# Optimization experiments

Measured on AMD Instinct MI355X. Metric: run time of the kernel, lower is better.

The kernel has to match this reference:

```python
import jax, jax.numpy as jnp
import numpy as np

IMG_C = 256
GC = 32  # graph_channel; must equal graph feature dim 32 for the residual


def setup_inputs() -> dict:
    key = jax.random.key(0)
    ks = jax.random.split(key, 10)
    B, N, WH_SIDE = 8, 4096, 64
    s = lambda fan_in: 1.0 / np.sqrt(fan_in)
    return {
        "input_graph": jax.random.normal(ks[0], (B, N, GC), jnp.float32),
        "input_image": jax.random.normal(ks[1], (B, IMG_C, WH_SIDE, WH_SIDE), jnp.float32),
        # Conv1d(kernel=1) weights stored as [out, in]
        "Wq": jax.random.uniform(ks[2], (GC, 32), jnp.float32, -s(32), s(32)),
        "bq": jax.random.uniform(ks[3], (GC,), jnp.float32, -s(32), s(32)),
        "Wk": jax.random.uniform(ks[4], (GC, IMG_C), jnp.float32, -s(IMG_C), s(IMG_C)),
        "bk": jax.random.uniform(ks[5], (GC,), jnp.float32, -s(IMG_C), s(IMG_C)),
        "Wv": jax.random.uniform(ks[6], (GC, IMG_C), jnp.float32, -s(IMG_C), s(IMG_C)),
        "bv": jax.random.uniform(ks[7], (GC,), jnp.float32, -s(IMG_C), s(IMG_C)),
        "Wc": jax.random.uniform(ks[8], (GC, GC), jnp.float32, -s(GC), s(GC)),
        "bc": jax.random.uniform(ks[9], (GC,), jnp.float32, -s(GC), s(GC)),
    }


def reference(input_graph, input_image, Wq, bq, Wk, bk, Wv, bv, Wc, bc):
    B, C, W, H = input_image.shape
    img = input_image.reshape(B, C, W * H)                      # [B, C, L]
    # 1x1 conv projections == channel matmuls
    K = jnp.einsum('oc,bcl->bol', Wk, img) + bk[None, :, None]  # [B, GC, L]
    V = jnp.einsum('oc,bcl->bol', Wv, img) + bv[None, :, None]  # [B, GC, L]
    # Q: graph [B, N, 32] -> conv over channel dim -> [B, N, GC]
    Q = jnp.einsum('oc,bnc->bno', Wq, input_graph) + bq[None, None, :]
    att = jnp.einsum('bno,bol->bnl', Q, K) / jnp.sqrt(jnp.float32(GC))  # [B, N, L]
    # NOTE: original softmax is over dim=1 (the node/query axis)
    att = jax.nn.softmax(att, axis=1)
    message = jnp.einsum('bol,bnl->bon', V, att)                # [B, GC, N]
    out = input_graph.transpose(0, 2, 1) + (
        jnp.einsum('oc,bcn->bon', Wc, message) + bc[None, :, None]
    )                                                           # [B, GC, N]
    return out.transpose(0, 2, 1)                               # [B, N, GC]
```

## Files before the change

kernel.cpp:

```cpp
#include <hip/hip_runtime.h>

#define BB 8
#define NN 4096
#define LL 4096
#define CC 256

typedef short bf16x8 __attribute__((ext_vector_type(8)));
typedef _Float16 f16x8 __attribute__((ext_vector_type(8)));
typedef __fp16 hf16x2 __attribute__((ext_vector_type(2)));
typedef float f32x4 __attribute__((ext_vector_type(4)));

__device__ __forceinline__ float bf2f(short s) {
  union { unsigned u; float f; } v;
  v.u = ((unsigned)(unsigned short)s) << 16;
  return v.f;
}
__device__ __forceinline__ short f2bf(float f) {
  union { float f; unsigned u; } v; v.f = f;
  unsigned r = v.u + 0x7fffu + ((v.u >> 16) & 1u);
  return (short)(r >> 16);
}

__device__ __forceinline__ int detect_f32(const void* g) {
  const unsigned* u = (const unsigned*)g;
  int cnt = 0;
  #pragma unroll
  for (int i = 0; i < 64; ++i) {
    unsigned e = (u[i] >> 23) & 0xffu;
    cnt += (e >= 100u && e <= 140u) ? 1 : 0;
  }
  return cnt >= 32;
}

__device__ __forceinline__ float ldel(const void* p, size_t i, int f32m) {
  return f32m ? ((const float*)p)[i] : bf2f(((const short*)p)[i]);
}
__device__ __forceinline__ bf16x8 ld8bf(const void* p, size_t i, int f32m) {
  if (f32m) {
    const float* fp = (const float*)p + i;
    float4 a = *(const float4*)fp;
    float4 b = *(const float4*)(fp + 4);
    bf16x8 r;
    r[0] = f2bf(a.x); r[1] = f2bf(a.y); r[2] = f2bf(a.z); r[3] = f2bf(a.w);
    r[4] = f2bf(b.x); r[5] = f2bf(b.y); r[6] = f2bf(b.z); r[7] = f2bf(b.w);
    return r;
  }
  return *(const bf16x8*)((const short*)p + i);
}

__global__ __launch_bounds__(256) void ka_proj(
    const void* __restrict__ graph, const void* __restrict__ img,
    const void* __restrict__ Wq, const void* __restrict__ bq,
    const void* __restrict__ Wk, const void* __restrict__ bk,
    const void* __restrict__ Wv, const void* __restrict__ bv,
    short* __restrict__ Qb, short* __restrict__ Kt, _Float16* __restrict__ Vt)
{
  const int f32m = detect_f32(graph);
  const int tid = threadIdx.x;
  const int w = tid >> 6, lane = tid & 63, lo = lane & 15, q = lane >> 4;
  const int bid = blockIdx.x;
  if (bid < 512) {
    const int b = bid >> 6;
    const int lt = ((bid & 63) << 6) + (w << 4);
    f32x4 aK0 = {0,0,0,0}, aK1 = {0,0,0,0}, aV0 = {0,0,0,0}, aV1 = {0,0,0,0};
    const size_t ibase = (size_t)b * CC * LL + lt + lo;
    #pragma unroll
    for (int cs = 0; cs < 8; ++cs) {
      const int c0 = cs * 32 + q * 8;
      bf16x8 bi;
      #pragma unroll
      for (int j = 0; j < 8; ++j)
        bi[j] = f2bf(ldel(img, ibase + (size_t)(c0 + j) * LL, f32m));
      bf16x8 wk0 = ld8bf(Wk, (size_t)lo * CC + c0, f32m);
      bf16x8 wk1 = ld8bf(Wk, (size_t)(lo + 16) * CC + c0, f32m);
      bf16x8 wv0 = ld8bf(Wv, (size_t)lo * CC + c0, f32m);
      bf16x8 wv1 = ld8bf(Wv, (size_t)(lo + 16) * CC + c0, f32m);
      aK0 = __builtin_amdgcn_mfma_f32_16x16x32_bf16(wk0, bi, aK0, 0, 0, 0);
      aK1 = __builtin_amdgcn_mfma_f32_16x16x32_bf16(wk1, bi, aK1, 0, 0, 0);
      aV0 = __builtin_amdgcn_mfma_f32_16x16x32_bf16(wv0, bi, aV0, 0, 0, 0);
      aV1 = __builtin_amdgcn_mfma_f32_16x16x32_bf16(wv1, bi, aV1, 0, 0, 0);
    }
    const float kscale = 0.2550348663f;
    const size_t row = ((size_t)b * LL + lt + lo) * 32;
    short4 s0, s1;
    s0.x = f2bf((aK0[0] + ldel(bk, q * 4 + 0, f32m)) * kscale);
    s0.y = f2bf((aK0[1] + ldel(bk, q * 4 + 1, f32m)) * kscale);
    s0.z = f2bf((aK0[2] + ldel(bk, q * 4 + 2, f32m)) * kscale);
    s0.w = f2bf((aK0[3] + ldel(bk, q * 4 + 3, f32m)) * kscale);
    s1.x = f2bf((aK1[0] + ldel(bk, 16 + q * 4 + 0, f32m)) * kscale);
    s1.y = f2bf((aK1[1] + ldel(bk, 16 + q * 4 + 1, f32m)) * kscale);
    s1.z = f2bf((aK1[2] + ldel(bk, 16 + q * 4 + 2, f32m)) * kscale);
    s1.w = f2bf((aK1[3] + ldel(bk, 16 + q * 4 + 3, f32m)) * kscale);
    *(short4*)(Kt + row + q * 4) = s0;
    *(short4*)(Kt + row + 16 + q * 4) = s1;
    union { hf16x2 h[2]; uint2 u; } p0, p1;
    p0.h[0] = __builtin_amdgcn_cvt_pkrtz(aV0[0] + ldel(bv, q * 4 + 0, f32m),
                                         aV0[1] + ldel(bv, q * 4 + 1, f32m));
    p0.h[1] = __builtin_amdgcn_cvt_pkrtz(aV0[2] + ldel(bv, q * 4 + 2, f32m),
                                         aV0[3] + ldel(bv, q * 4 + 3, f32m));
    p1.h[0] = __builtin_amdgcn_cvt_pkrtz(aV1[0] + ldel(bv, 16 + q * 4 + 0, f32m),
                                         aV1[1] + ldel(bv, 16 + q * 4 + 1, f32m));
    p1.h[1] = __builtin_amdgcn_cvt_pkrtz(aV1[2] + ldel(bv, 16 + q * 4 + 2, f32m),
                                         aV1[3] + ldel(bv, 16 + q * 4 + 3, f32m));
    *(uint2*)(Vt + row + q * 4) = p0.u;
    *(uint2*)(Vt + row + 16 + q * 4) = p1.u;
  } else {
    const int t = bid - 512;
    const int b = t >> 6;
    const int nt = ((t & 63) << 6) + (w << 4);
    bf16x8 ag = ld8bf(graph, ((size_t)b * NN + nt + lo) * 32 + q * 8, f32m);
    bf16x8 w0 = ld8bf(Wq, (size_t)lo * 32 + q * 8, f32m);
    bf16x8 w1 = ld8bf(Wq, (size_t)(lo + 16) * 32 + q * 8, f32m);
    f32x4 z = {0,0,0,0};
    f32x4 a0 = __builtin_amdgcn_mfma_f32_16x16x32_bf16(ag, w0, z, 0, 0, 0);
    f32x4 a1 = __builtin_amdgcn_mfma_f32_16x16x32_bf16(ag, w1, z, 0, 0, 0);
    const float b0 = ldel(bq, lo, f32m), b1 = ldel(bq, lo + 16, f32m);
    #pragma unroll
    for (int r = 0; r < 4; ++r) {
      const size_t rowq = ((size_t)b * NN + nt + q * 4 + r) * 32;
      Qb[rowq + lo] = f2bf(a0[r] + b0);
      Qb[rowq + 16 + lo] = f2bf(a1[r] + b1);
    }
  }
}

__global__ __launch_bounds__(256) void kb_z(
    const short* __restrict__ Qb, const short* __restrict__ Kt,
    const _Float16* __restrict__ Vt, _Float16* __restrict__ Vpp)
{
  __shared__ float zpart[4][64];
  __shared__ float zinv[64];
  const int tid = threadIdx.x;
  const int w = tid >> 6, lane = tid & 63, lo = lane & 15, q = lane >> 4;
  const int b = blockIdx.x >> 6;
  const int l0 = (blockIdx.x & 63) << 6;
  bf16x8 kf[4];
  #pragma unroll
  for (int f = 0; f < 4; ++f)
    kf[f] = *(const bf16x8*)(Kt + ((size_t)b * LL + l0 + f * 16 + lo) * 32 + q * 8);
  float za[4][4] = {{0}};
  const short* qbase = Qb + ((size_t)b * NN + w * 1024 + lo) * 32 + q * 8;
  for (int it = 0; it < 64; ++it) {
    bf16x8 qf = *(const bf16x8*)(qbase + it * 512);
    #pragma unroll
    for (int f = 0; f < 4; ++f) {
      f32x4 z = {0,0,0,0};
      f32x4 c = __builtin_amdgcn_mfma_f32_16x16x32_bf16(kf[f], qf, z, 0, 0, 0);
      #pragma unroll
      for (int r = 0; r < 4; ++r) za[f][r] += __builtin_exp2f(c[r]);
    }
  }
  #pragma unroll
  for (int m = 1; m < 16; m <<= 1)
    #pragma unroll
    for (int f = 0; f < 4; ++f)
      #pragma unroll
      for (int r = 0; r < 4; ++r)
        za[f][r] += __shfl_xor(za[f][r], m, 64);
  if (lo == 0) {
    #pragma unroll
    for (int f = 0; f < 4; ++f)
      #pragma unroll
      for (int r = 0; r < 4; ++r)
        zpart[w][f * 16 + q * 4 + r] = za[f][r];
  }
  __syncthreads();
  if (tid < 64) {
    const float z = zpart[0][tid] + zpart[1][tid] + zpart[2][tid] + zpart[3][tid];
    zinv[tid] = 4096.0f / z;
  }
  __syncthreads();
  {
    const int l = tid & 63, og = tid >> 6;
    const float inv = zinv[l];
    const f16x8 vv = *(const f16x8*)(Vt + ((size_t)b * LL + l0 + l) * 32 + og * 8);
    #pragma unroll
    for (int j = 0; j < 8; ++j) {
      const float sv = (float)vv[j] * inv;
      Vpp[((size_t)b * 32 + og * 8 + j) * LL + l0 + l] = (_Float16)sv;
    }
  }
}

__global__ __launch_bounds__(256) void kc_attn(
    const short* __restrict__ Qb, const short* __restrict__ Kt,
    const _Float16* __restrict__ Vpp, const void* __restrict__ graph,
    const void* __restrict__ Wc, const void* __restrict__ bc,
    void* __restrict__ outv)
{
  __shared__ __align__(16) _Float16 P[4][32][72];
  __shared__ __align__(16) float msgL[4][32][36];
  const int f32m = detect_f32(graph);
  const int tid = threadIdx.x;
  const int w = tid >> 6, lane = tid & 63, lo = lane & 15, q = lane >> 4;
  const int b = blockIdx.x >> 7;
  const int n0 = (blockIdx.x & 127) << 5;
  const bf16x8 qf0 = *(const bf16x8*)(Qb + ((size_t)b * NN + n0 + lo) * 32 + q * 8);
  const bf16x8 qf1 = *(const bf16x8*)(Qb + ((size_t)b * NN + n0 + 16 + lo) * 32 + q * 8);
  f32x4 m00 = {0,0,0,0}, m01 = {0,0,0,0}, m10 = {0,0,0,0}, m11 = {0,0,0,0};
  const short* ktb = Kt + (size_t)b * LL * 32 + lo * 32 + q * 8;
  const _Float16* vb0 = Vpp + ((size_t)b * 32 + lo) * LL;
  const _Float16* vb1 = vb0 + (size_t)16 * LL;
  for (int lc = w * 16; lc < w * 16 + 16; ++lc) {
    const int lbase = lc * 64;
    #pragma unroll
    for (int f = 0; f < 4; ++f) {
      bf16x8 kf = *(const bf16x8*)(ktb + (size_t)(lbase + f * 16) * 32);
      f32x4 z = {0,0,0,0};
      f32x4 c0 = __builtin_amdgcn_mfma_f32_16x16x32_bf16(kf, qf0, z, 0, 0, 0);
      f32x4 c1 = __builtin_amdgcn_mfma_f32_16x16x32_bf16(kf, qf1, z, 0, 0, 0);
      union { hf16x2 h[2]; uint2 u; } pk0, pk1;
      pk0.h[0] = __builtin_amdgcn_cvt_pkrtz(__builtin_exp2f(c0[0]), __builtin_exp2f(c0[1]));
      pk0.h[1] = __builtin_amdgcn_cvt_pkrtz(__builtin_exp2f(c0[2]), __builtin_exp2f(c0[3]));
      pk1.h[0] = __builtin_amdgcn_cvt_pkrtz(__builtin_exp2f(c1[0]), __builtin_exp2f(c1[1]));
      pk1.h[1] = __builtin_amdgcn_cvt_pkrtz(__builtin_exp2f(c1[2]), __builtin_exp2f(c1[3]));
      *(uint2*)&P[w][lo][f * 16 + q * 4] = pk0.u;
      *(uint2*)&P[w][16 + lo][f * 16 + q * 4] = pk1.u;
    }
    #pragma unroll
    for (int k = 0; k < 2; ++k) {
      f16x8 pa0 = *(const f16x8*)&P[w][lo][k * 32 + q * 8];
      f16x8 pa1 = *(const f16x8*)&P[w][16 + lo][k * 32 + q * 8];
      f16x8 v0 = *(const f16x8*)(vb0 + lbase + k * 32 + q * 8);
      f16x8 v1 = *(const f16x8*)(vb1 + lbase + k * 32 + q * 8);
      m00 = __builtin_amdgcn_mfma_f32_16x16x32_f16(pa0, v0, m00, 0, 0, 0);
      m01 = __builtin_amdgcn_mfma_f32_16x16x32_f16(pa0, v1, m01, 0, 0, 0);
      m10 = __builtin_amdgcn_mfma_f32_16x16x32_f16(pa1, v0, m10, 0, 0, 0);
      m11 = __builtin_amdgcn_mfma_f32_16x16x32_f16(pa1, v1, m11, 0, 0, 0);
    }
  }
  #pragma unroll
  for (int r = 0; r < 4; ++r) {
    msgL[w][q * 4 + r][lo] = m00[r];
    msgL[w][q * 4 + r][16 + lo] = m01[r];
    msgL[w][16 + q * 4 + r][lo] = m10[r];
    msgL[w][16 + q * 4 + r][16 + lo] = m11[r];
  }
  __syncthreads();
  const int o = lane & 31, nh = lane >> 5;
  float wcr[32];
  #pragma unroll
  for (int c4 = 0; c4 < 8; ++c4)
    #pragma unroll
    for (int jj = 0; jj < 4; ++jj)
      wcr[c4 * 4 + jj] = ldel(Wc, o * 32 + c4 * 4 + jj, f32m) * (1.0f / 4096.0f);
  const float bcv = ldel(bc, o, f32m);
  #pragma unroll
  for (int rr = 0; rr < 4; ++rr) {
    const int nl = w * 8 + nh * 4 + rr;
    f32x4 s = {0,0,0,0};
    #pragma unroll
    for (int cc = 0; cc < 8; ++cc) {
      f32x4 ma = *(const f32x4*)&msgL[0][nl][cc * 4];
      f32x4 mb = *(const f32x4*)&msgL[1][nl][cc * 4];
      f32x4 mc = *(const f32x4*)&msgL[2][nl][cc * 4];
      f32x4 md = *(const f32x4*)&msgL[3][nl][cc * 4];
      f32x4 m4 = ma + mb + mc + md;
      s[0] += wcr[cc * 4 + 0] * m4[0];
      s[1] += wcr[cc * 4 + 1] * m4[1];
      s[2] += wcr[cc * 4 + 2] * m4[2];
      s[3] += wcr[cc * 4 + 3] * m4[3];
    }
    const size_t idx = ((size_t)b * NN + n0 + nl) * 32 + o;
    const float val = s[0] + s[1] + s[2] + s[3] + bcv + ldel(graph, idx, f32m);
    if (f32m) ((float*)outv)[idx] = val;
    else      ((short*)outv)[idx] = f2bf(val);
  }
}

extern "C" void kernel_launch(void* const* d_in, const int* in_sizes, int n_in,
                              void* d_out, int out_size, void* d_ws, size_t ws_size,
                              hipStream_t stream) {
  const void* graph = d_in[0];
  const void* img   = d_in[1];
  const void* Wq    = d_in[2];
  const void* bq    = d_in[3];
  const void* Wk    = d_in[4];
  const void* bk    = d_in[5];
  const void* Wv    = d_in[6];
  const void* bv    = d_in[7];
  const void* Wc    = d_in[8];
  const void* bc    = d_in[9];
  char* ws = (char*)d_ws;
  short*    Qb  = (short*)(ws + 0);
  short*    Kt  = (short*)(ws + 2097152);
  _Float16* Vt  = (_Float16*)(ws + 4194304);
  _Float16* Vpp = (_Float16*)(ws + 6291456);
  ka_proj<<<dim3(1024), dim3(256), 0, stream>>>(graph, img, Wq, bq, Wk, bk, Wv, bv,
                                                Qb, Kt, Vt);
  kb_z<<<dim3(512), dim3(256), 0, stream>>>(Qb, Kt, Vt, Vpp);
  kc_attn<<<dim3(1024), dim3(256), 0, stream>>>(Qb, Kt, Vpp, graph, Wc, bc, d_out);
}
```

Measured before the change: 218.4 us.

## Drop dtype detection, widen column-sum kernel to 1024 threads, use raw exp2

Removes the runtime fp32/bf16 detection and branching loads, hard-coding fp32 inputs so each kernel skips the 64-word probe and the per-element branch. The normalizer kernel now runs 16 waves per block, each summing over a quarter of the previous node range, which gives more parallelism in the exp-sum pass. Exp calls switch to the raw hardware exp2 builtin, dropping the library wrapper's range handling. The bf16 input path is lost, and the raw exp2 may handle denormal or edge inputs differently.

```diff
diff --git a/kernel.cpp b/kernel.cpp
--- a/kernel.cpp
+++ b/kernel.cpp
@@ -7,55 +7,31 @@
 
 typedef short bf16x8 __attribute__((ext_vector_type(8)));
 typedef _Float16 f16x8 __attribute__((ext_vector_type(8)));
+typedef _Float16 f16x2 __attribute__((ext_vector_type(2)));
 typedef __fp16 hf16x2 __attribute__((ext_vector_type(2)));
 typedef float f32x4 __attribute__((ext_vector_type(4)));
 
-__device__ __forceinline__ float bf2f(short s) {
-  union { unsigned u; float f; } v;
-  v.u = ((unsigned)(unsigned short)s) << 16;
-  return v.f;
-}
 __device__ __forceinline__ short f2bf(float f) {
   union { float f; unsigned u; } v; v.f = f;
   unsigned r = v.u + 0x7fffu + ((v.u >> 16) & 1u);
   return (short)(r >> 16);
 }
-
-__device__ __forceinline__ int detect_f32(const void* g) {
-  const unsigned* u = (const unsigned*)g;
-  int cnt = 0;
-  #pragma unroll
-  for (int i = 0; i < 64; ++i) {
-    unsigned e = (u[i] >> 23) & 0xffu;
-    cnt += (e >= 100u && e <= 140u) ? 1 : 0;
-  }
-  return cnt >= 32;
-}
-
-__device__ __forceinline__ float ldel(const void* p, size_t i, int f32m) {
-  return f32m ? ((const float*)p)[i] : bf2f(((const short*)p)[i]);
-}
-__device__ __forceinline__ bf16x8 ld8bf(const void* p, size_t i, int f32m) {
-  if (f32m) {
-    const float* fp = (const float*)p + i;
-    float4 a = *(const float4*)fp;
-    float4 b = *(const float4*)(fp + 4);
-    bf16x8 r;
-    r[0] = f2bf(a.x); r[1] = f2bf(a.y); r[2] = f2bf(a.z); r[3] = f2bf(a.w);
-    r[4] = f2bf(b.x); r[5] = f2bf(b.y); r[6] = f2bf(b.z); r[7] = f2bf(b.w);
-    return r;
-  }
-  return *(const bf16x8*)((const short*)p + i);
+__device__ __forceinline__ bf16x8 ld8(const float* __restrict__ fp) {
+  float4 a = *(const float4*)fp;
+  float4 b = *(const float4*)(fp + 4);
+  bf16x8 r;
+  r[0] = f2bf(a.x); r[1] = f2bf(a.y); r[2] = f2bf(a.z); r[3] = f2bf(a.w);
+  r[4] = f2bf(b.x); r[5] = f2bf(b.y); r[6] = f2bf(b.z); r[7] = f2bf(b.w);
+  return r;
 }
 
 __global__ __launch_bounds__(256) void ka_proj(
-    const void* __restrict__ graph, const void* __restrict__ img,
-    const void* __restrict__ Wq, const void* __restrict__ bq,
-    const void* __restrict__ Wk, const void* __restrict__ bk,
-    const void* __restrict__ Wv, const void* __restrict__ bv,
+    const float* __restrict__ graph, const float* __restrict__ img,
+    const float* __restrict__ Wq, const float* __restrict__ bq,
+    const float* __restrict__ Wk, const float* __restrict__ bk,
+    const float* __restrict__ Wv, const float* __restrict__ bv,
     short* __restrict__ Qb, short* __restrict__ Kt, _Float16* __restrict__ Vt)
 {
-  const int f32m = detect_f32(graph);
   const int tid = threadIdx.x;
   const int w = tid >> 6, lane = tid & 63, lo = lane & 15, q = lane >> 4;
   const int bid = blockIdx.x;
@@ -63,18 +39,17 @@
     const int b = bid >> 6;
     const int lt = ((bid & 63) << 6) + (w << 4);
     f32x4 aK0 = {0,0,0,0}, aK1 = {0,0,0,0}, aV0 = {0,0,0,0}, aV1 = {0,0,0,0};
-    const size_t ibase = (size_t)b * CC * LL + lt + lo;
+    const float* ib = img + (size_t)b * CC * LL + lt + lo;
     #pragma unroll
     for (int cs = 0; cs < 8; ++cs) {
       const int c0 = cs * 32 + q * 8;
       bf16x8 bi;
       #pragma unroll
-      for (int j = 0; j < 8; ++j)
-        bi[j] = f2bf(ldel(img, ibase + (size_t)(c0 + j) * LL, f32m));
-      bf16x8 wk0 = ld8bf(Wk, (size_t)lo * CC + c0, f32m);
-      bf16x8 wk1 = ld8bf(Wk, (size_t)(lo + 16) * CC + c0, f32m);
-      bf16x8 wv0 = ld8bf(Wv, (size_t)lo * CC + c0, f32m);
-      bf16x8 wv1 = ld8bf(Wv, (size_t)(lo + 16) * CC + c0, f32m);
+      for (int j = 0; j < 8; ++j) bi[j] = f2bf(ib[(size_t)(c0 + j) * LL]);
+      bf16x8 wk0 = ld8(Wk + lo * CC + c0);
+      bf16x8 wk1 = ld8(Wk + (lo + 16) * CC + c0);
+      bf16x8 wv0 = ld8(Wv + lo * CC + c0);
+      bf16x8 wv1 = ld8(Wv + (lo + 16) * CC + c0);
       aK0 = __builtin_amdgcn_mfma_f32_16x16x32_bf16(wk0, bi, aK0, 0, 0, 0);
       aK1 = __builtin_amdgcn_mfma_f32_16x16x32_bf16(wk1, bi, aK1, 0, 0, 0);
       aV0 = __builtin_amdgcn_mfma_f32_16x16x32_bf16(wv0, bi, aV0, 0, 0, 0);
@@ -83,38 +58,34 @@
     const float kscale = 0.2550348663f;
     const size_t row = ((size_t)b * LL + lt + lo) * 32;
     short4 s0, s1;
-    s0.x = f2bf((aK0[0] + ldel(bk, q * 4 + 0, f32m)) * kscale);
-    s0.y = f2bf((aK0[1] + ldel(bk, q * 4 + 1, f32m)) * kscale);
-    s0.z = f2bf((aK0[2] + ldel(bk, q * 4 + 2, f32m)) * kscale);
-    s0.w = f2bf((aK0[3] + ldel(bk, q * 4 + 3, f32m)) * kscale);
-    s1.x = f2bf((aK1[0] + ldel(bk, 16 + q * 4 + 0, f32m)) * kscale);
-    s1.y = f2bf((aK1[1] + ldel(bk, 16 + q * 4 + 1, f32m)) * kscale);
-    s1.z = f2bf((aK1[2] + ldel(bk, 16 + q * 4 + 2, f32m)) * kscale);
-    s1.w = f2bf((aK1[3] + ldel(bk, 16 + q * 4 + 3, f32m)) * kscale);
+    s0.x = f2bf((aK0[0] + bk[q * 4 + 0]) * kscale);
+    s0.y = f2bf((aK0[1] + bk[q * 4 + 1]) * kscale);
+    s0.z = f2bf((aK0[2] + bk[q * 4 + 2]) * kscale);
+    s0.w = f2bf((aK0[3] + bk[q * 4 + 3]) * kscale);
+    s1.x = f2bf((aK1[0] + bk[16 + q * 4 + 0]) * kscale);
+    s1.y = f2bf((aK1[1] + bk[16 + q * 4 + 1]) * kscale);
+    s1.z = f2bf((aK1[2] + bk[16 + q * 4 + 2]) * kscale);
+    s1.w = f2bf((aK1[3] + bk[16 + q * 4 + 3]) * kscale);
     *(short4*)(Kt + row + q * 4) = s0;
     *(short4*)(Kt + row + 16 + q * 4) = s1;
     union { hf16x2 h[2]; uint2 u; } p0, p1;
-    p0.h[0] = __builtin_amdgcn_cvt_pkrtz(aV0[0] + ldel(bv, q * 4 + 0, f32m),
-                                         aV0[1] + ldel(bv, q * 4 + 1, f32m));
-    p0.h[1] = __builtin_amdgcn_cvt_pkrtz(aV0[2] + ldel(bv, q * 4 + 2, f32m),
-                                         aV0[3] + ldel(bv, q * 4 + 3, f32m));
-    p1.h[0] = __builtin_amdgcn_cvt_pkrtz(aV1[0] + ldel(bv, 16 + q * 4 + 0, f32m),
-                                         aV1[1] + ldel(bv, 16 + q * 4 + 1, f32m));
-    p1.h[1] = __builtin_amdgcn_cvt_pkrtz(aV1[2] + ldel(bv, 16 + q * 4 + 2, f32m),
-                                         aV1[3] + ldel(bv, 16 + q * 4 + 3, f32m));
+    p0.h[0] = __builtin_amdgcn_cvt_pkrtz(aV0[0] + bv[q * 4 + 0], aV0[1] + bv[q * 4 + 1]);
+    p0.h[1] = __builtin_amdgcn_cvt_pkrtz(aV0[2] + bv[q * 4 + 2], aV0[3] + bv[q * 4 + 3]);
+    p1.h[0] = __builtin_amdgcn_cvt_pkrtz(aV1[0] + bv[16 + q * 4 + 0], aV1[1] + bv[16 + q * 4 + 1]);
+    p1.h[1] = __builtin_amdgcn_cvt_pkrtz(aV1[2] + bv[16 + q * 4 + 2], aV1[3] + bv[16 + q * 4 + 3]);
     *(uint2*)(Vt + row + q * 4) = p0.u;
     *(uint2*)(Vt + row + 16 + q * 4) = p1.u;
   } else {
     const int t = bid - 512;
     const int b = t >> 6;
     const int nt = ((t & 63) << 6) + (w << 4);
-    bf16x8 ag = ld8bf(graph, ((size_t)b * NN + nt + lo) * 32 + q * 8, f32m);
-    bf16x8 w0 = ld8bf(Wq, (size_t)lo * 32 + q * 8, f32m);
-    bf16x8 w1 = ld8bf(Wq, (size_t)(lo + 16) * 32 + q * 8, f32m);
+    bf16x8 ag = ld8(graph + ((size_t)b * NN + nt + lo) * 32 + q * 8);
+    bf16x8 w0 = ld8(Wq + lo * 32 + q * 8);
+    bf16x8 w1 = ld8(Wq + (lo + 16) * 32 + q * 8);
     f32x4 z = {0,0,0,0};
     f32x4 a0 = __builtin_amdgcn_mfma_f32_16x16x32_bf16(ag, w0, z, 0, 0, 0);
     f32x4 a1 = __builtin_amdgcn_mfma_f32_16x16x32_bf16(ag, w1, z, 0, 0, 0);
-    const float b0 = ldel(bq, lo, f32m), b1 = ldel(bq, lo + 16, f32m);
+    const float b0 = bq[lo], b1 = bq[lo + 16];
     #pragma unroll
     for (int r = 0; r < 4; ++r) {
       const size_t rowq = ((size_t)b * NN + nt + q * 4 + r) * 32;
@@ -124,11 +95,11 @@
   }
 }
 
-__global__ __launch_bounds__(256) void kb_z(
+__global__ __launch_bounds__(1024) void kb_z(
     const short* __restrict__ Qb, const short* __restrict__ Kt,
     const _Float16* __restrict__ Vt, _Float16* __restrict__ Vpp)
 {
-  __shared__ float zpart[4][64];
+  __shared__ float zpart[16][64];
   __shared__ float zinv[64];
   const int tid = threadIdx.x;
   const int w = tid >> 6, lane = tid & 63, lo = lane & 15, q = lane >> 4;
@@ -139,15 +110,15 @@
   for (int f = 0; f < 4; ++f)
     kf[f] = *(const bf16x8*)(Kt + ((size_t)b * LL + l0 + f * 16 + lo) * 32 + q * 8);
   float za[4][4] = {{0}};
-  const short* qbase = Qb + ((size_t)b * NN + w * 1024 + lo) * 32 + q * 8;
-  for (int it = 0; it < 64; ++it) {
+  const short* qbase = Qb + ((size_t)b * NN + w * 256 + lo) * 32 + q * 8;
+  for (int it = 0; it < 16; ++it) {
     bf16x8 qf = *(const bf16x8*)(qbase + it * 512);
     #pragma unroll
     for (int f = 0; f < 4; ++f) {
       f32x4 z = {0,0,0,0};
       f32x4 c = __builtin_amdgcn_mfma_f32_16x16x32_bf16(kf[f], qf, z, 0, 0, 0);
       #pragma unroll
-      for (int r = 0; r < 4; ++r) za[f][r] += __builtin_exp2f(c[r]);
+      for (int r = 0; r < 4; ++r) za[f][r] += __builtin_amdgcn_exp2f(c[r]);
     }
   }
   #pragma unroll
@@ -166,31 +137,29 @@
   }
   __syncthreads();
   if (tid < 64) {
-    const float z = zpart[0][tid] + zpart[1][tid] + zpart[2][tid] + zpart[3][tid];
+    float z = 0.f;
+    #pragma unroll
+    for (int t = 0; t < 16; ++t) z += zpart[t][tid];
     zinv[tid] = 4096.0f / z;
   }
   __syncthreads();
   {
     const int l = tid & 63, og = tid >> 6;
     const float inv = zinv[l];
-    const f16x8 vv = *(const f16x8*)(Vt + ((size_t)b * LL + l0 + l) * 32 + og * 8);
-    #pragma unroll
-    for (int j = 0; j < 8; ++j) {
-      const float sv = (float)vv[j] * inv;
-      Vpp[((size_t)b * 32 + og * 8 + j) * LL + l0 + l] = (_Float16)sv;
-    }
+    const f16x2 vv = *(const f16x2*)(Vt + ((size_t)b * LL + l0 + l) * 32 + og * 2);
+    Vpp[((size_t)b * 32 + og * 2 + 0) * LL + l0 + l] = (_Float16)((float)vv[0] * inv);
+    Vpp[((size_t)b * 32 + og * 2 + 1) * LL + l0 + l] = (_Float16)((float)vv[1] * inv);
   }
 }
 
 __global__ __launch_bounds__(256) void kc_attn(
     const short* __restrict__ Qb, const short* __restrict__ Kt,
-    const _Float16* __restrict__ Vpp, const void* __restrict__ graph,
-    const void* __restrict__ Wc, const void* __restrict__ bc,
-    void* __restrict__ outv)
+    const _Float16* __restrict__ Vpp, const float* __restrict__ graph,
+    const float* __restrict__ Wc, const float* __restrict__ bc,
+    float* __restrict__ out)
 {
   __shared__ __align__(16) _Float16 P[4][32][72];
   __shared__ __align__(16) float msgL[4][32][36];
-  const int f32m = detect_f32(graph);
   const int tid = threadIdx.x;
   const int w = tid >> 6, lane = tid & 63, lo = lane & 15, q = lane >> 4;
   const int b = blockIdx.x >> 7;
@@ -210,10 +179,14 @@
       f32x4 c0 = __builtin_amdgcn_mfma_f32_16x16x32_bf16(kf, qf0, z, 0, 0, 0);
       f32x4 c1 = __builtin_amdgcn_mfma_f32_16x16x32_bf16(kf, qf1, z, 0, 0, 0);
       union { hf16x2 h[2]; uint2 u; } pk0, pk1;
-      pk0.h[0] = __builtin_amdgcn_cvt_pkrtz(__builtin_exp2f(c0[0]), __builtin_exp2f(c0[1]));
-      pk0.h[1] = __builtin_amdgcn_cvt_pkrtz(__builtin_exp2f(c0[2]), __builtin_exp2f(c0[3]));
-      pk1.h[0] = __builtin_amdgcn_cvt_pkrtz(__builtin_exp2f(c1[0]), __builtin_exp2f(c1[1]));
-      pk1.h[1] = __builtin_amdgcn_cvt_pkrtz(__builtin_exp2f(c1[2]), __builtin_exp2f(c1[3]));
+      pk0.h[0] = __builtin_amdgcn_cvt_pkrtz(__builtin_amdgcn_exp2f(c0[0]),
+                                            __builtin_amdgcn_exp2f(c0[1]));
+      pk0.h[1] = __builtin_amdgcn_cvt_pkrtz(__builtin_amdgcn_exp2f(c0[2]),
+                                            __builtin_amdgcn_exp2f(c0[3]));
+      pk1.h[0] = __builtin_amdgcn_cvt_pkrtz(__builtin_amdgcn_exp2f(c1[0]),
+                                            __builtin_amdgcn_exp2f(c1[1]));
+      pk1.h[1] = __builtin_amdgcn_cvt_pkrtz(__builtin_amdgcn_exp2f(c1[2]),
+                                            __builtin_amdgcn_exp2f(c1[3]));
       *(uint2*)&P[w][lo][f * 16 + q * 4] = pk0.u;
       *(uint2*)&P[w][16 + lo][f * 16 + q * 4] = pk1.u;
     }
@@ -240,11 +213,14 @@
   const int o = lane & 31, nh = lane >> 5;
   float wcr[32];
   #pragma unroll
-  for (int c4 = 0; c4 < 8; ++c4)
-    #pragma unroll
-    for (int jj = 0; jj < 4; ++jj)
-      wcr[c4 * 4 + jj] = ldel(Wc, o * 32 + c4 * 4 + jj, f32m) * (1.0f / 4096.0f);
-  const float bcv = ldel(bc, o, f32m);
+  for (int c4 = 0; c4 < 8; ++c4) {
+    float4 wc4 = *(const float4*)(Wc + o * 32 + c4 * 4);
+    wcr[c4 * 4 + 0] = wc4.x * (1.0f / 4096.0f);
+    wcr[c4 * 4 + 1] = wc4.y * (1.0f / 4096.0f);
+    wcr[c4 * 4 + 2] = wc4.z * (1.0f / 4096.0f);
+    wcr[c4 * 4 + 3] = wc4.w * (1.0f / 4096.0f);
+  }
+  const float bcv = bc[o];
   #pragma unroll
   for (int rr = 0; rr < 4; ++rr) {
     const int nl = w * 8 + nh * 4 + rr;
@@ -262,25 +238,23 @@
       s[3] += wcr[cc * 4 + 3] * m4[3];
     }
     const size_t idx = ((size_t)b * NN + n0 + nl) * 32 + o;
-    const float val = s[0] + s[1] + s[2] + s[3] + bcv + ldel(graph, idx, f32m);
-    if (f32m) ((float*)outv)[idx] = val;
-    else      ((short*)outv)[idx] = f2bf(val);
+    out[idx] = s[0] + s[1] + s[2] + s[3] + bcv + graph[idx];
   }
 }
 
 extern "C" void kernel_launch(void* const* d_in, const int* in_sizes, int n_in,
                               void* d_out, int out_size, void* d_ws, size_t ws_size,
                               hipStream_t stream) {
-  const void* graph = d_in[0];
-  const void* img   = d_in[1];
-  const void* Wq    = d_in[2];
-  const void* bq    = d_in[3];
-  const void* Wk    = d_in[4];
-  const void* bk    = d_in[5];
-  const void* Wv    = d_in[6];
-  const void* bv    = d_in[7];
-  const void* Wc    = d_in[8];
-  const void* bc    = d_in[9];
+  const float* graph = (const float*)d_in[0];
+  const float* img   = (const float*)d_in[1];
+  const float* Wq    = (const float*)d_in[2];
+  const float* bq    = (const float*)d_in[3];
+  const float* Wk    = (const float*)d_in[4];
+  const float* bk    = (const float*)d_in[5];
+  const float* Wv    = (const float*)d_in[6];
+  const float* bv    = (const float*)d_in[7];
+  const float* Wc    = (const float*)d_in[8];
+  const float* bc    = (const float*)d_in[9];
   char* ws = (char*)d_ws;
   short*    Qb  = (short*)(ws + 0);
   short*    Kt  = (short*)(ws + 2097152);
@@ -288,6 +262,7 @@
   _Float16* Vpp = (_Float16*)(ws + 6291456);
   ka_proj<<<dim3(1024), dim3(256), 0, stream>>>(graph, img, Wq, bq, Wk, bk, Wv, bv,
                                                 Qb, Kt, Vt);
-  kb_z<<<dim3(512), dim3(256), 0, stream>>>(Qb, Kt, Vt, Vpp);
-  kc_attn<<<dim3(1024), dim3(256), 0, stream>>>(Qb, Kt, Vpp, graph, Wc, bc, d_out);
-}
+  kb_z<<<dim3(512), dim3(1024), 0, stream>>>(Qb, Kt, Vt, Vpp);
+  kc_attn<<<dim3(1024), dim3(256), 0, stream>>>(Qb, Kt, Vpp, graph, Wc, bc,
+                                                (float*)d_out);
+}
```

Result: faster. 209.2 us (-4.2%).
